# Kernel tuning notes

Measured on AMD Instinct MI355X. Metric: run time of the kernel, lower is better.

## Reference

```python
import jax, jax.numpy as jnp
import numpy as np

G = 1024  # max number of groups per batch row (max_group_length in the torch code)


def setup_inputs() -> dict:
    key = jax.random.key(0)
    k1, k2 = jax.random.split(key)
    B, S, H = 8, 8192, 512
    feats = jax.random.normal(k1, (B, S, H), dtype=jnp.float32)
    # sorted segment ids encode the ragged List[List[int]] group sizes:
    # segment_ids[b, s] = index of the group token s belongs to, non-decreasing in s
    segment_ids = jnp.sort(jax.random.randint(k2, (B, S), 0, G, dtype=jnp.int32), axis=-1)
    return {"feats": feats, "segment_ids": segment_ids}


def reference(feats, segment_ids):
    """Segment mean-pooling: equivalent to bmm(sparse COO weights, feats)
    where weights[b, j, s] = 1/len(group_j) for tokens s in group j.
    Returns (grouped [B, G, H], group_lengths [B, G])."""
    B, S, H = feats.shape
    # offset ids so each batch row owns a disjoint segment range -> one flat segment_sum
    flat_ids = (segment_ids + jnp.arange(B, dtype=segment_ids.dtype)[:, None] * G).reshape(-1)
    sums = jax.ops.segment_sum(feats.reshape(B * S, H), flat_ids,
                               num_segments=B * G).reshape(B, G, H)
    counts = jax.ops.segment_sum(jnp.ones((B * S,), dtype=feats.dtype), flat_ids,
                                 num_segments=B * G).reshape(B, G)
    # mean aggregation (pow = -1): each token weighted by 1/group_len, i.e. sum/count.
    # empty groups produce zero rows, matching zero rows of the sparse bmm.
    grouped = sums / jnp.maximum(counts, 1.0)[..., None]
    return grouped, counts.astype(jnp.int32)
```

## Files before the change

### kernel.cpp

```cpp
#include <hip/hip_runtime.h>

#define BB 8
#define SS 8192
#define HH 512
#define GG 1024
#define GPB 4

typedef float f32x4 __attribute__((ext_vector_type(4)));

__global__ __launch_bounds__(256) void seg_offsets_kernel(
    const int* __restrict__ ids,
    int*       __restrict__ offsets)
{
    const int tid = blockIdx.x * 256 + threadIdx.x;
    const int b = tid / SS;
    const int s = tid - b * SS;
    const int* __restrict__ row = ids + (size_t)b * SS;
    int* __restrict__ offs = offsets + (size_t)b * (GG + 1);

    const int cur  = row[s];
    const int prev = (s > 0) ? row[s - 1] : -1;
    for (int g = prev + 1; g <= cur; ++g) offs[g] = s;
    if (s == SS - 1) {
        for (int g = cur + 1; g <= GG; ++g) offs[g] = SS;
    }
}

__global__ __launch_bounds__(128) void group_mean_kernel(
    const f32x4* __restrict__ feats,
    const int*   __restrict__ offsets,
    f32x4*       __restrict__ grouped,
    float*       __restrict__ counts)
{
    const int g0 = blockIdx.x * GPB;
    const int b  = blockIdx.y;
    const int t  = threadIdx.x;

    const int* __restrict__ offs = offsets + (size_t)b * (GG + 1) + g0;
    int o[GPB + 1];
    #pragma unroll
    for (int i = 0; i < GPB + 1; ++i) o[i] = offs[i];

    const f32x4* __restrict__ fb = feats + (size_t)b * SS * (HH / 4);

    #pragma unroll
    for (int i = 0; i < GPB; ++i) {
        const int lo = o[i], hi = o[i + 1];
        const int n = hi - lo;
        f32x4 a0 = 0.f, a1 = 0.f, a2 = 0.f, a3 = 0.f;
        int s = lo;
        for (; s + 3 < hi; s += 4) {
            f32x4 v0 = __builtin_nontemporal_load(&fb[(size_t)(s    ) * (HH / 4) + t]);
            f32x4 v1 = __builtin_nontemporal_load(&fb[(size_t)(s + 1) * (HH / 4) + t]);
            f32x4 v2 = __builtin_nontemporal_load(&fb[(size_t)(s + 2) * (HH / 4) + t]);
            f32x4 v3 = __builtin_nontemporal_load(&fb[(size_t)(s + 3) * (HH / 4) + t]);
            a0 += v0; a1 += v1; a2 += v2; a3 += v3;
        }
        for (; s < hi; ++s) {
            a0 += __builtin_nontemporal_load(&fb[(size_t)s * (HH / 4) + t]);
        }
        const float inv = (n > 0) ? (1.0f / (float)n) : 0.0f;
        f32x4 r = ((a0 + a1) + (a2 + a3)) * inv;
        __builtin_nontemporal_store(r, &grouped[((size_t)b * GG + g0 + i) * (HH / 4) + t]);
        if (t == 0) counts[(size_t)b * GG + g0 + i] = (float)n;
    }
}

extern "C" void kernel_launch(void* const* d_in, const int* in_sizes, int n_in,
                              void* d_out, int out_size, void* d_ws, size_t ws_size,
                              hipStream_t stream) {
    const float* feats = (const float*)d_in[0];
    const int*   ids   = (const int*)d_in[1];
    float* grouped = (float*)d_out;
    float* counts  = grouped + (size_t)BB * GG * HH;
    int*   offsets = (int*)d_ws;

    seg_offsets_kernel<<<(BB * SS) / 256, 256, 0, stream>>>(ids, offsets);
    dim3 grid(GG / GPB, BB);
    group_mean_kernel<<<grid, 128, 0, stream>>>((const f32x4*)feats, offsets,
                                                (f32x4*)grouped, counts);
}
```

Baseline: 189.4 us.

## Partition work by fixed token chunks with atomic merge of boundary groups

Replaces the per-group work split with fixed 64-token chunks per block, so every block streams the same number of rows regardless of group sizes. Groups that cross chunk boundaries are combined with float atomic adds into an output that is zeroed beforehand, and counts move to a separate small kernel. This targets load imbalance from variable group sizes. The cost is two extra launches, a full zero pass over the output, atomic traffic on boundary groups, and results that can vary slightly between runs because the atomic adds land in no fixed order.

```diff
diff --git a/kernel.cpp b/kernel.cpp
--- a/kernel.cpp
+++ b/kernel.cpp
@@ -4,7 +4,7 @@
 #define SS 8192
 #define HH 512
 #define GG 1024
-#define GPB 4
+#define CHUNK 64
 
 typedef float f32x4 __attribute__((ext_vector_type(4)));
 
@@ -26,43 +26,67 @@
     }
 }
 
-__global__ __launch_bounds__(128) void group_mean_kernel(
+__global__ __launch_bounds__(256) void zero_kernel(f32x4* __restrict__ p) {
+    const size_t i = (size_t)blockIdx.x * 256 + threadIdx.x;
+    __builtin_nontemporal_store((f32x4)0.f, &p[i]);
+}
+
+__global__ __launch_bounds__(256) void counts_kernel(
+    const int* __restrict__ offsets, float* __restrict__ counts) {
+    const int i = blockIdx.x * 256 + threadIdx.x;
+    const int b = i >> 10, g = i & (GG - 1);
+    const int* offs = offsets + (size_t)b * (GG + 1);
+    counts[i] = (float)(offs[g + 1] - offs[g]);
+}
+
+__global__ __launch_bounds__(128) void group_mean_chunk_kernel(
     const f32x4* __restrict__ feats,
+    const int*   __restrict__ ids,
     const int*   __restrict__ offsets,
-    f32x4*       __restrict__ grouped,
-    float*       __restrict__ counts)
+    float*       __restrict__ grouped)
 {
-    const int g0 = blockIdx.x * GPB;
-    const int b  = blockIdx.y;
-    const int t  = threadIdx.x;
+    const int c = blockIdx.x;
+    const int b = blockIdx.y;
+    const int t = threadIdx.x;
+    const int s0 = c * CHUNK, s1 = s0 + CHUNK;
 
-    const int* __restrict__ offs = offsets + (size_t)b * (GG + 1) + g0;
-    int o[GPB + 1];
-    #pragma unroll
-    for (int i = 0; i < GPB + 1; ++i) o[i] = offs[i];
-
+    const int* __restrict__ offs = offsets + (size_t)b * (GG + 1);
     const f32x4* __restrict__ fb = feats + (size_t)b * SS * (HH / 4);
 
-    #pragma unroll
-    for (int i = 0; i < GPB; ++i) {
-        const int lo = o[i], hi = o[i + 1];
-        const int n = hi - lo;
-        f32x4 a0 = 0.f, a1 = 0.f, a2 = 0.f, a3 = 0.f;
-        int s = lo;
-        for (; s + 3 < hi; s += 4) {
-            f32x4 v0 = __builtin_nontemporal_load(&fb[(size_t)(s    ) * (HH / 4) + t]);
-            f32x4 v1 = __builtin_nontemporal_load(&fb[(size_t)(s + 1) * (HH / 4) + t]);
-            f32x4 v2 = __builtin_nontemporal_load(&fb[(size_t)(s + 2) * (HH / 4) + t]);
-            f32x4 v3 = __builtin_nontemporal_load(&fb[(size_t)(s + 3) * (HH / 4) + t]);
-            a0 += v0; a1 += v1; a2 += v2; a3 += v3;
+    int g   = ids[(size_t)b * SS + s0];
+    int cur = offs[g];
+    while (cur < s1) {
+        const int nxt = offs[g + 1];
+        const int rl = cur > s0 ? cur : s0;
+        const int rh = nxt < s1 ? nxt : s1;
+        if (rh > rl) {
+            const int n = nxt - cur;
+            const float inv = 1.0f / (float)n;
+            f32x4 a0 = 0.f, a1 = 0.f, a2 = 0.f, a3 = 0.f;
+            int s = rl;
+            for (; s + 3 < rh; s += 4) {
+                f32x4 v0 = __builtin_nontemporal_load(&fb[(size_t)(s    ) * (HH / 4) + t]);
+                f32x4 v1 = __builtin_nontemporal_load(&fb[(size_t)(s + 1) * (HH / 4) + t]);
+                f32x4 v2 = __builtin_nontemporal_load(&fb[(size_t)(s + 2) * (HH / 4) + t]);
+                f32x4 v3 = __builtin_nontemporal_load(&fb[(size_t)(s + 3) * (HH / 4) + t]);
+                a0 += v0; a1 += v1; a2 += v2; a3 += v3;
+            }
+            for (; s < rh; ++s)
+                a0 += __builtin_nontemporal_load(&fb[(size_t)s * (HH / 4) + t]);
+            const f32x4 r = ((a0 + a1) + (a2 + a3)) * inv;
+
+            float* __restrict__ orow =
+                grouped + ((size_t)b * GG + g) * HH + t * 4;
+            if (cur >= s0 && nxt <= s1) {
+                *(f32x4*)orow = r;
+            } else {
+                unsafeAtomicAdd(orow + 0, r.x);
+                unsafeAtomicAdd(orow + 1, r.y);
+                unsafeAtomicAdd(orow + 2, r.z);
+                unsafeAtomicAdd(orow + 3, r.w);
+            }
         }
-        for (; s < hi; ++s) {
-            a0 += __builtin_nontemporal_load(&fb[(size_t)s * (HH / 4) + t]);
-        }
-        const float inv = (n > 0) ? (1.0f / (float)n) : 0.0f;
-        f32x4 r = ((a0 + a1) + (a2 + a3)) * inv;
-        __builtin_nontemporal_store(r, &grouped[((size_t)b * GG + g0 + i) * (HH / 4) + t]);
-        if (t == 0) counts[(size_t)b * GG + g0 + i] = (float)n;
+        cur = nxt; ++g;
     }
 }
 
@@ -75,8 +99,11 @@
     float* counts  = grouped + (size_t)BB * GG * HH;
     int*   offsets = (int*)d_ws;
 
+    zero_kernel<<<(BB * GG * (HH / 4)) / 256, 256, 0, stream>>>((f32x4*)grouped);
     seg_offsets_kernel<<<(BB * SS) / 256, 256, 0, stream>>>(ids, offsets);
-    dim3 grid(GG / GPB, BB);
-    group_mean_kernel<<<grid, 128, 0, stream>>>((const f32x4*)feats, offsets,
-                                                (f32x4*)grouped, counts);
+    counts_kernel<<<(BB * GG) / 256, 256, 0, stream>>>(offsets, counts);
+
+    dim3 grid(SS / CHUNK, BB);
+    group_mean_chunk_kernel<<<grid, 128, 0, stream>>>(
+        (const f32x4*)feats, ids, offsets, grouped);
 }
```

After: 204.9 us. 1.08x slower.
